# Kernel optimization log

Hardware: AMD Instinct MI355X
Metric: run time of the kernel (lower is better)

## Reference

```python
import jax, jax.numpy as jnp
import numpy as np

STRIDES = (8, 16, 32)
REG_MAX = 16
NUM_CLASSES = 80
FMP = ((80, 80), (40, 40), (20, 20))  # 640x640 input / strides


def _anchors(h, w, stride):
    # torch.meshgrid([arange(h), arange(w)]) -> (y, x); stack [x, y]; +0.5; *stride
    ys, xs = jnp.meshgrid(jnp.arange(h, dtype=jnp.float32),
                          jnp.arange(w, dtype=jnp.float32), indexing='ij')
    return (jnp.stack([xs, ys], axis=-1).reshape(-1, 2) + 0.5) * stride  # [H*W, 2]


def _level(cls_feat, reg_feat, cls_w, cls_b, reg_w, reg_b, stride):
    B, _, H, W = cls_feat.shape
    M = H * W
    # 1x1 convs as channel contractions, directly producing NHWC layout
    cls_pred = jnp.einsum('bchw,oc->bhwo', cls_feat, cls_w) + cls_b  # [B,H,W,nc]
    reg_pred = jnp.einsum('bchw,oc->bhwo', reg_feat, reg_w) + reg_b  # [B,H,W,4*reg_max]
    cls_pred = cls_pred.reshape(B, M, NUM_CLASSES)
    reg_pred = reg_pred.reshape(B, M, 4, REG_MAX)
    # DFL: softmax over reg_max bins, project with linspace(0, reg_max, reg_max)
    proj = jnp.linspace(0.0, float(REG_MAX), REG_MAX)
    reg = jnp.einsum('bmfr,r->bmf', jax.nn.softmax(reg_pred, axis=-1), proj)  # [B,M,4]
    anch = _anchors(H, W, stride)  # [M,2], broadcasts over B
    box = jnp.concatenate([anch - reg[..., :2] * stride,
                           anch + reg[..., 2:] * stride], axis=-1)  # [B,M,4]
    return jnp.concatenate([jax.nn.sigmoid(cls_pred), box], axis=-1)  # [B,M,nc+4]


def setup_inputs() -> dict:
    key = jax.random.key(0)
    ks = jax.random.split(key, 18)
    d = {}
    for i, (h, w) in enumerate(FMP):
        d[f'cls_feat{i}'] = jax.random.normal(ks[i], (16, 256, h, w), dtype=jnp.float32)
        d[f'reg_feat{i}'] = jax.random.normal(ks[3 + i], (16, 256, h, w), dtype=jnp.float32)
        d[f'cls_w{i}'] = jax.random.normal(ks[6 + i], (NUM_CLASSES, 256), dtype=jnp.float32) * 0.02
        d[f'cls_b{i}'] = jax.random.normal(ks[9 + i], (NUM_CLASSES,), dtype=jnp.float32) * 0.02
        d[f'reg_w{i}'] = jax.random.normal(ks[12 + i], (4 * REG_MAX, 256), dtype=jnp.float32) * 0.02
        d[f'reg_b{i}'] = jax.random.normal(ks[15 + i], (4 * REG_MAX,), dtype=jnp.float32) * 0.02
    return d


def reference(cls_feat0, cls_feat1, cls_feat2,
              reg_feat0, reg_feat1, reg_feat2,
              cls_w0, cls_w1, cls_w2, cls_b0, cls_b1, cls_b2,
              reg_w0, reg_w1, reg_w2, reg_b0, reg_b1, reg_b2):
    cls_feats = (cls_feat0, cls_feat1, cls_feat2)
    reg_feats = (reg_feat0, reg_feat1, reg_feat2)
    cls_ws = (cls_w0, cls_w1, cls_w2)
    cls_bs = (cls_b0, cls_b1, cls_b2)
    reg_ws = (reg_w0, reg_w1, reg_w2)
    reg_bs = (reg_b0, reg_b1, reg_b2)
    outs = [_level(cls_feats[l], reg_feats[l], cls_ws[l], cls_bs[l],
                   reg_ws[l], reg_bs[l], STRIDES[l]) for l in range(3)]
    return jnp.concatenate(outs, axis=1)  # [B, 8400, nc+4]
```

## Files before the change

kernel.cpp:

```cpp
#include <hip/hip_runtime.h>
#include <hip/hip_bf16.h>
#include <cstdint>

typedef float v4f __attribute__((ext_vector_type(4)));
typedef float v2f __attribute__((ext_vector_type(2)));

#define LVL_WSTRIDE 40960
#define BIASPAD_OFF 122880

__global__ __launch_bounds__(256) void prep_weights(
    const float* __restrict__ cw0, const float* __restrict__ cb0,
    const float* __restrict__ rw0, const float* __restrict__ rb0,
    const float* __restrict__ cw1, const float* __restrict__ cb1,
    const float* __restrict__ rw1, const float* __restrict__ rb1,
    const float* __restrict__ cw2, const float* __restrict__ cb2,
    const float* __restrict__ rw2, const float* __restrict__ rb2,
    float* __restrict__ ws)
{
  const int gid = blockIdx.x * 256 + threadIdx.x;
  const float* cws[3] = {cw0, cw1, cw2};
  const float* cbs[3] = {cb0, cb1, cb2};
  const float* rws[3] = {rw0, rw1, rw2};
  const float* rbs[3] = {rb0, rb1, rb2};
  if (gid < 3 * LVL_WSTRIDE) {
    const int l = gid / LVL_WSTRIDE;
    const int rem = gid - l * LVL_WSTRIDE;
    const int c = rem / 160;
    const int j = rem - c * 160;
    float v = 0.f;
    if (j < 96) {
      const int g = j / 12, q = j - g * 12;
      if (q < 10) v = cws[l][(g * 10 + q) * 256 + c];
    } else {
      v = rws[l][(j - 96) * 256 + c];
    }
    ws[gid] = v;
  } else if (gid < 3 * LVL_WSTRIDE + 480) {
    const int i = gid - 3 * LVL_WSTRIDE;
    const int l = i / 160;
    const int j = i - l * 160;
    float v = 0.f;
    if (j < 96) {
      const int g = j / 12, q = j - g * 12;
      if (q < 10) v = cbs[l][g * 10 + q];
    } else {
      v = rbs[l][j - 96];
    }
    ws[BIASPAD_OFF + i] = v;
  }
}

__global__ __launch_bounds__(256, 3) void head_kernel(
    const float* __restrict__ cf0, const float* __restrict__ rf0,
    const float* __restrict__ cf1, const float* __restrict__ rf1,
    const float* __restrict__ cf2, const float* __restrict__ rf2,
    const float* __restrict__ ws, float* __restrict__ out)
{
  __shared__ float pool[11008];
  float* const As     = pool;
  float* const Bs     = pool + 1024;
  float* const rstage = pool + 1792;
  float* const dstage = pool + 10496;
  float* const ostage = pool;

  const int t = threadIdx.x;
  const int bid = blockIdx.x;

  int l, r;
  if (bid < 800)       { l = 0; r = bid; }
  else if (bid < 1008) { l = 1; r = bid - 800; }
  else                 { l = 2; r = bid - 1008; }

  const int tiles = (l == 0) ? 50 : (l == 1) ? 13 : 4;
  const int M     = (l == 0) ? 6400 : (l == 1) ? 1600 : 400;
  const int W     = (l == 0) ? 80 : (l == 1) ? 40 : 20;
  const int moff  = (l == 0) ? 0 : (l == 1) ? 6400 : 8000;
  const float sv  = (float)(8 << l);

  const int b    = r / tiles;
  const int tile = r - b * tiles;
  const int m0   = tile * 128;

  const float* const cf   = (l == 0) ? cf0 : (l == 1) ? cf1 : cf2;
  const float* const rf   = (l == 0) ? rf0 : (l == 1) ? rf1 : rf2;
  const float* const wT   = ws + l * LVL_WSTRIDE;
  const float* const bias = ws + BIASPAD_OFF + l * 160;

  const int mg  = t & 31;
  const int og  = t >> 5;
  const int mg4 = mg * 4;

  const int mclamp = min(m0 + mg4, M - 4);

  float accR[4][8];
#pragma unroll
  for (int i = 0; i < 4; ++i)
#pragma unroll
    for (int j = 0; j < 8; ++j) accR[i][j] = 0.f;

  const float* const featR = rf + (size_t)b * 256 * (size_t)M;
  for (int ks = 0; ks < 32; ++ks) {
    const int k = ks * 8;
    const v4f av = *(const v4f*)(featR + (size_t)(k + og) * M + mclamp);
    v4f bv;
    if (t < 128) {
      const int cc = t >> 4, jj = (t & 15) * 4;
      bv = *(const v4f*)(wT + (k + cc) * 160 + 96 + jj);
    }
    __syncthreads();
    *(v4f*)&As[t * 4] = av;
    if (t < 128) *(v4f*)&Bs[t * 4] = bv;
    __syncthreads();
#pragma unroll
    for (int cc = 0; cc < 8; ++cc) {
      const v4f a  = *(const v4f*)&As[cc * 128 + mg4];
      const v4f b0 = *(const v4f*)&Bs[cc * 64 + og * 8];
      const v4f b1 = *(const v4f*)&Bs[cc * 64 + og * 8 + 4];
#pragma unroll
      for (int i = 0; i < 4; ++i) {
#pragma unroll
        for (int j = 0; j < 4; ++j) {
          accR[i][j]     += a[i] * b0[j];
          accR[i][j + 4] += a[i] * b1[j];
        }
      }
    }
  }
  __syncthreads();

#pragma unroll
  for (int i = 0; i < 4; ++i) {
    const int m = mg4 + i;
#pragma unroll
    for (int j = 0; j < 8; ++j)
      rstage[m * 68 + og * 8 + j] = accR[i][j] + bias[96 + og * 8 + j];
  }
  __syncthreads();

  float dv0 = 0.f, dv1 = 0.f;
#pragma unroll
  for (int it = 0; it < 2; ++it) {
    const int tau = t + it * 256;
    const int m = tau >> 2, f = tau & 3;
    const float* xp = &rstage[m * 68 + f * 16];
    float x[16];
    *(v4f*)&x[0]  = *(const v4f*)(xp);
    *(v4f*)&x[4]  = *(const v4f*)(xp + 4);
    *(v4f*)&x[8]  = *(const v4f*)(xp + 8);
    *(v4f*)&x[12] = *(const v4f*)(xp + 12);
    float mx = x[0];
#pragma unroll
    for (int q = 1; q < 16; ++q) mx = fmaxf(mx, x[q]);
    float s = 0.f, d = 0.f;
#pragma unroll
    for (int q = 0; q < 16; ++q) {
      const float e = __expf(x[q] - mx);
      s += e;
      d += e * (float)q;
    }
    const float res = d * (16.f / 15.f) / s;
    if (it == 0) dv0 = res; else dv1 = res;
  }
  dstage[t]       = dv0;
  dstage[t + 256] = dv1;
  __syncthreads();

  float bx0 = 0.f, by0 = 0.f, bx1 = 0.f, by1 = 0.f;
  if (t < 128) {
    const v4f dd = *(const v4f*)&dstage[t * 4];
    const int mglob = m0 + t;
    const int hh = mglob / W;
    const int wcol = mglob - hh * W;
    const float ax = ((float)wcol + 0.5f) * sv;
    const float ay = ((float)hh + 0.5f) * sv;
    bx0 = ax - dd[0] * sv;
    by0 = ay - dd[1] * sv;
    bx1 = ax + dd[2] * sv;
    by1 = ay + dd[3] * sv;
  }

  float accC[4][10];
#pragma unroll
  for (int i = 0; i < 4; ++i)
#pragma unroll
    for (int j = 0; j < 10; ++j) accC[i][j] = 0.f;

  const float* const featC = cf + (size_t)b * 256 * (size_t)M;
  for (int ks = 0; ks < 32; ++ks) {
    const int k = ks * 8;
    const v4f av = *(const v4f*)(featC + (size_t)(k + og) * M + mclamp);
    v4f bv;
    if (t < 192) {
      const int cc = t / 24;
      const int jj = (t - cc * 24) * 4;
      bv = *(const v4f*)(wT + (k + cc) * 160 + jj);
    }
    __syncthreads();
    *(v4f*)&As[t * 4] = av;
    if (t < 192) *(v4f*)&Bs[t * 4] = bv;
    __syncthreads();
#pragma unroll
    for (int cc = 0; cc < 8; ++cc) {
      const v4f a  = *(const v4f*)&As[cc * 128 + mg4];
      const v4f b0 = *(const v4f*)&Bs[cc * 96 + og * 12];
      const v4f b1 = *(const v4f*)&Bs[cc * 96 + og * 12 + 4];
      const v2f b2 = *(const v2f*)&Bs[cc * 96 + og * 12 + 8];
#pragma unroll
      for (int i = 0; i < 4; ++i) {
#pragma unroll
        for (int j = 0; j < 4; ++j) {
          accC[i][j]     += a[i] * b0[j];
          accC[i][j + 4] += a[i] * b1[j];
        }
        accC[i][8] += a[i] * b2[0];
        accC[i][9] += a[i] * b2[1];
      }
    }
  }
  __syncthreads();

#pragma unroll
  for (int i = 0; i < 4; ++i) {
    const int m = mg4 + i;
#pragma unroll
    for (int j = 0; j < 10; ++j) {
      const float z = accC[i][j] + bias[og * 12 + j];
      ostage[m * 84 + og * 10 + j] = 1.f / (1.f + __expf(-z));
    }
  }
  if (t < 128) {
    v4f bb; bb[0] = bx0; bb[1] = by0; bb[2] = bx1; bb[3] = by1;
    *(v4f*)&ostage[t * 84 + 80] = bb;
  }
  __syncthreads();

  float* const obase = out + ((size_t)b * 8400 + moff + m0) * 84;
#pragma unroll
  for (int i = 0; i < 21; ++i) {
    const int p  = i * 256 + t;
    const int fe = p * 2;
    const int m  = fe / 84;
    if (m0 + m < M) {
      *(v2f*)(obase + fe) = *(const v2f*)&ostage[fe];
    }
  }
}

extern "C" void kernel_launch(void* const* d_in, const int* in_sizes, int n_in,
                              void* d_out, int out_size, void* d_ws, size_t ws_size,
                              hipStream_t stream) {
  const float* cf[3]; const float* rff[3];
  const float* cw[3]; const float* cb[3];
  const float* rw[3]; const float* rb[3];
  for (int i = 0; i < 3; ++i) {
    cf[i]  = (const float*)d_in[i * 6 + 0];
    rff[i] = (const float*)d_in[i * 6 + 1];
    cw[i]  = (const float*)d_in[i * 6 + 2];
    cb[i]  = (const float*)d_in[i * 6 + 3];
    rw[i]  = (const float*)d_in[i * 6 + 4];
    rb[i]  = (const float*)d_in[i * 6 + 5];
  }
  float* ws = (float*)d_ws;
  float* o  = (float*)d_out;

  prep_weights<<<dim3(482), dim3(256), 0, stream>>>(
      cw[0], cb[0], rw[0], rb[0],
      cw[1], cb[1], rw[1], rb[1],
      cw[2], cb[2], rw[2], rb[2], ws);

  head_kernel<<<dim3(1072), dim3(256), 0, stream>>>(
      cf[0], rff[0], cf[1], rff[1], cf[2], rff[2], ws, o);
}
```

Baseline: 399.7 us.

## Use split-bf16 MFMA for 1x1 conv GEMMs with shuffle-based DFL softmax

Replaces the scalar FP32 FMA GEMMs with MFMA 16x16x32 bf16 instructions. Each FP32 operand is split into hi and lo bf16 parts and three MFMAs per tile keep accuracy close to FP32. Weights are pre-swizzled into MFMA lane order by the prep kernel. Feature loads are software-prefetched one k-slice ahead, and the DFL softmax now runs in registers with cross-lane shuffles, which removes the LDS staging passes. The cost is extra ALU work to pack the hi/lo parts and a small precision loss from the dropped lo*lo term. The kernel is likely memory-bound on roughly 300MB of feature reads.

Result: faster. 352.9 us (-11.7%).

```diff
diff --git a/kernel.cpp b/kernel.cpp
--- a/kernel.cpp
+++ b/kernel.cpp
@@ -4,9 +4,30 @@
 
 typedef float v4f __attribute__((ext_vector_type(4)));
 typedef float v2f __attribute__((ext_vector_type(2)));
-
-#define LVL_WSTRIDE 40960
-#define BIASPAD_OFF 122880
+typedef short s8v __attribute__((ext_vector_type(8)));
+typedef unsigned short u16;
+
+#define WSB_LVL     73728
+#define WSB_CLS_SZ  40960
+#define BIAS_OFF_B  442368
+
+__device__ __forceinline__ u16 bfbits(float x) {
+  return __builtin_bit_cast(u16, __float2bfloat16(x));
+}
+__device__ __forceinline__ float bff(u16 b) {
+  return __builtin_bit_cast(float, ((unsigned int)b) << 16);
+}
+__device__ __forceinline__ unsigned int packhi(float a, float b) {
+  return (unsigned int)bfbits(a) | ((unsigned int)bfbits(b) << 16);
+}
+__device__ __forceinline__ unsigned int packlo(float a, float b) {
+  const float ra = a - bff(bfbits(a));
+  const float rb = b - bff(bfbits(b));
+  return packhi(ra, rb);
+}
+__device__ __forceinline__ v4f mfma16(s8v a, s8v b, v4f c) {
+  return __builtin_amdgcn_mfma_f32_16x16x32_bf16(a, b, c, 0, 0, 0);
+}
 
 __global__ __launch_bounds__(256) void prep_weights(
     const float* __restrict__ cw0, const float* __restrict__ cb0,
@@ -15,38 +36,103 @@
     const float* __restrict__ rw1, const float* __restrict__ rb1,
     const float* __restrict__ cw2, const float* __restrict__ cb2,
     const float* __restrict__ rw2, const float* __restrict__ rb2,
-    float* __restrict__ ws)
+    void* __restrict__ wsv)
 {
+  u16* wsB = (u16*)wsv;
+  float* biasf = (float*)((char*)wsv + BIAS_OFF_B);
   const int gid = blockIdx.x * 256 + threadIdx.x;
   const float* cws[3] = {cw0, cw1, cw2};
   const float* cbs[3] = {cb0, cb1, cb2};
   const float* rws[3] = {rw0, rw1, rw2};
   const float* rbs[3] = {rb0, rb1, rb2};
-  if (gid < 3 * LVL_WSTRIDE) {
-    const int l = gid / LVL_WSTRIDE;
-    const int rem = gid - l * LVL_WSTRIDE;
-    const int c = rem / 160;
-    const int j = rem - c * 160;
-    float v = 0.f;
-    if (j < 96) {
-      const int g = j / 12, q = j - g * 12;
-      if (q < 10) v = cws[l][(g * 10 + q) * 256 + c];
-    } else {
-      v = rws[l][(j - 96) * 256 + c];
-    }
-    ws[gid] = v;
-  } else if (gid < 3 * LVL_WSTRIDE + 480) {
-    const int i = gid - 3 * LVL_WSTRIDE;
-    const int l = i / 160;
-    const int j = i - l * 160;
-    float v = 0.f;
-    if (j < 96) {
-      const int g = j / 12, q = j - g * 12;
-      if (q < 10) v = cbs[l][g * 10 + q];
-    } else {
-      v = rbs[l][j - 96];
-    }
-    ws[BIASPAD_OFF + i] = v;
+
+  if (gid < 3 * WSB_LVL) {
+    const int l = gid / WSB_LVL;
+    int r = gid - l * WSB_LVL;
+    const bool cls = r < WSB_CLS_SZ;
+    if (!cls) r -= WSB_CLS_SZ;
+    const int j    = r & 7;
+    const int lane = (r >> 3) & 63;
+    const int hl   = (r >> 9) & 1;
+    int nt, ks;
+    if (cls) { const int v = r >> 10; nt = v % 5; ks = v / 5; }
+    else     { nt = (r >> 10) & 3; ks = r >> 12; }
+    const int o = nt * 16 + (lane & 15);
+    const int k = ks * 32 + (lane >> 4) * 8 + j;
+    const float* w = cls ? cws[l] : rws[l];
+    const float v = w[o * 256 + k];
+    u16 bits;
+    if (hl == 0) bits = bfbits(v);
+    else         bits = bfbits(v - bff(bfbits(v)));
+    wsB[gid] = bits;
+  } else if (gid < 3 * WSB_LVL + 432) {
+    const int i = gid - 3 * WSB_LVL;
+    const int l = i / 144;
+    const int o = i - l * 144;
+    biasf[l * 144 + o] = (o < 80) ? cbs[l][o] : rbs[l][o - 80];
+  }
+}
+
+template<int NT>
+__device__ __forceinline__ void gemm_accum(const float* __restrict__ feat,
+                                           const u16* __restrict__ wB,
+                                           u16* Abuf, const int t,
+                                           const int m0, const int M,
+                                           v4f (&acc)[2][NT])
+{
+  const int kp   = t & 15;
+  const int mq0  = t >> 4;
+  const int mmA  = min(m0 + mq0 * 4, M - 4);
+  const int mmB  = min(m0 + (mq0 + 16) * 4, M - 4);
+  const int lane   = t & 63;
+  const int lane15 = lane & 15;
+  const int kg     = lane >> 4;
+  const int mbase  = (t >> 6) * 32;
+  unsigned int* AbufW = (unsigned int*)Abuf;
+  const int w0 = (mq0 * 4) * 36 + kp;
+  const int w1 = ((mq0 + 16) * 4) * 36 + kp;
+
+  v4f r0a = *(const v4f*)(feat + (size_t)(2 * kp) * M + mmA);
+  v4f r0b = *(const v4f*)(feat + (size_t)(2 * kp + 1) * M + mmA);
+  v4f r1a = *(const v4f*)(feat + (size_t)(2 * kp) * M + mmB);
+  v4f r1b = *(const v4f*)(feat + (size_t)(2 * kp + 1) * M + mmB);
+
+#pragma unroll
+  for (int ks = 0; ks < 8; ++ks) {
+#pragma unroll
+    for (int j = 0; j < 4; ++j) {
+      AbufW[w0 + j * 36]      = packhi(r0a[j], r0b[j]);
+      AbufW[w0 + j * 36 + 16] = packlo(r0a[j], r0b[j]);
+      AbufW[w1 + j * 36]      = packhi(r1a[j], r1b[j]);
+      AbufW[w1 + j * 36 + 16] = packlo(r1a[j], r1b[j]);
+    }
+    if (ks < 7) {
+      const size_t ko = (size_t)((ks + 1) * 32 + 2 * kp) * M;
+      r0a = *(const v4f*)(feat + ko + mmA);
+      r0b = *(const v4f*)(feat + ko + M + mmA);
+      r1a = *(const v4f*)(feat + ko + mmB);
+      r1b = *(const v4f*)(feat + ko + M + mmB);
+    }
+    __syncthreads();
+    const u16* arow0 = Abuf + (mbase + lane15) * 72 + kg * 8;
+    const u16* arow1 = Abuf + (mbase + 16 + lane15) * 72 + kg * 8;
+    const s8v ahi0 = *(const s8v*)(arow0);
+    const s8v alo0 = *(const s8v*)(arow0 + 32);
+    const s8v ahi1 = *(const s8v*)(arow1);
+    const s8v alo1 = *(const s8v*)(arow1 + 32);
+#pragma unroll
+    for (int nt = 0; nt < NT; ++nt) {
+      const u16* bp = wB + (size_t)((ks * NT + nt) * 2) * 512 + lane * 8;
+      const s8v bhi = *(const s8v*)(bp);
+      const s8v blo = *(const s8v*)(bp + 512);
+      acc[0][nt] = mfma16(ahi0, bhi, acc[0][nt]);
+      acc[0][nt] = mfma16(ahi0, blo, acc[0][nt]);
+      acc[0][nt] = mfma16(alo0, bhi, acc[0][nt]);
+      acc[1][nt] = mfma16(ahi1, bhi, acc[1][nt]);
+      acc[1][nt] = mfma16(ahi1, blo, acc[1][nt]);
+      acc[1][nt] = mfma16(alo1, bhi, acc[1][nt]);
+    }
+    __syncthreads();
   }
 }
 
@@ -54,16 +140,17 @@
     const float* __restrict__ cf0, const float* __restrict__ rf0,
     const float* __restrict__ cf1, const float* __restrict__ rf1,
     const float* __restrict__ cf2, const float* __restrict__ rf2,
-    const float* __restrict__ ws, float* __restrict__ out)
+    const void* __restrict__ wsv, float* __restrict__ out)
 {
-  __shared__ float pool[11008];
-  float* const As     = pool;
-  float* const Bs     = pool + 1024;
-  float* const rstage = pool + 1792;
-  float* const dstage = pool + 10496;
-  float* const ostage = pool;
-
-  const int t = threadIdx.x;
+  __shared__ __align__(16) char smem[45056];
+  u16*  Abuf     = (u16*)smem;
+  float* ostage   = (float*)smem;
+  float* boxstage = (float*)(smem + 43008);
+
+  const u16*  wsB   = (const u16*)wsv;
+  const float* biasf = (const float*)((const char*)wsv + BIAS_OFF_B);
+
+  const int t   = threadIdx.x;
   const int bid = blockIdx.x;
 
   int l, r;
@@ -81,155 +168,98 @@
   const int tile = r - b * tiles;
   const int m0   = tile * 128;
 
-  const float* const cf   = (l == 0) ? cf0 : (l == 1) ? cf1 : cf2;
-  const float* const rf   = (l == 0) ? rf0 : (l == 1) ? rf1 : rf2;
-  const float* const wT   = ws + l * LVL_WSTRIDE;
-  const float* const bias = ws + BIASPAD_OFF + l * 160;
-
-  const int mg  = t & 31;
-  const int og  = t >> 5;
-  const int mg4 = mg * 4;
-
-  const int mclamp = min(m0 + mg4, M - 4);
-
-  float accR[4][8];
-#pragma unroll
-  for (int i = 0; i < 4; ++i)
-#pragma unroll
-    for (int j = 0; j < 8; ++j) accR[i][j] = 0.f;
-
-  const float* const featR = rf + (size_t)b * 256 * (size_t)M;
-  for (int ks = 0; ks < 32; ++ks) {
-    const int k = ks * 8;
-    const v4f av = *(const v4f*)(featR + (size_t)(k + og) * M + mclamp);
-    v4f bv;
-    if (t < 128) {
-      const int cc = t >> 4, jj = (t & 15) * 4;
-      bv = *(const v4f*)(wT + (k + cc) * 160 + 96 + jj);
-    }
-    __syncthreads();
-    *(v4f*)&As[t * 4] = av;
-    if (t < 128) *(v4f*)&Bs[t * 4] = bv;
-    __syncthreads();
-#pragma unroll
-    for (int cc = 0; cc < 8; ++cc) {
-      const v4f a  = *(const v4f*)&As[cc * 128 + mg4];
-      const v4f b0 = *(const v4f*)&Bs[cc * 64 + og * 8];
-      const v4f b1 = *(const v4f*)&Bs[cc * 64 + og * 8 + 4];
-#pragma unroll
-      for (int i = 0; i < 4; ++i) {
-#pragma unroll
-        for (int j = 0; j < 4; ++j) {
-          accR[i][j]     += a[i] * b0[j];
-          accR[i][j + 4] += a[i] * b1[j];
-        }
+  const float* cfL = (l == 0) ? cf0 : (l == 1) ? cf1 : cf2;
+  const float* rfL = (l == 0) ? rf0 : (l == 1) ? rf1 : rf2;
+  const float* featR = rfL + (size_t)b * 256 * (size_t)M;
+  const float* featC = cfL + (size_t)b * 256 * (size_t)M;
+  const u16* wBcls = wsB + l * WSB_LVL;
+  const u16* wBreg = wsB + l * WSB_LVL + WSB_CLS_SZ;
+  const int loff = l * 144;
+
+  const int lane   = t & 63;
+  const int lane15 = lane & 15;
+  const int kg     = lane >> 4;
+  const int mbase  = (t >> 6) * 32;
+
+  v4f accR[2][4];
+#pragma unroll
+  for (int mr = 0; mr < 2; ++mr)
+#pragma unroll
+    for (int nt = 0; nt < 4; ++nt) accR[mr][nt] = (v4f){0.f, 0.f, 0.f, 0.f};
+  gemm_accum<4>(featR, wBreg, Abuf, t, m0, M, accR);
+
+  float bR[4];
+#pragma unroll
+  for (int f = 0; f < 4; ++f) bR[f] = biasf[loff + 80 + f * 16 + lane15];
+
+  float d[2][4][4];
+#pragma unroll
+  for (int mr = 0; mr < 2; ++mr) {
+#pragma unroll
+    for (int f = 0; f < 4; ++f) {
+#pragma unroll
+      for (int rr = 0; rr < 4; ++rr) {
+        const float xx = accR[mr][f][rr] + bR[f];
+        float mx = xx;
+        mx = fmaxf(mx, __shfl_xor(mx, 1));
+        mx = fmaxf(mx, __shfl_xor(mx, 2));
+        mx = fmaxf(mx, __shfl_xor(mx, 4));
+        mx = fmaxf(mx, __shfl_xor(mx, 8));
+        const float e = __expf(xx - mx);
+        float s = e, wq = e * (float)lane15;
+        s += __shfl_xor(s, 1); wq += __shfl_xor(wq, 1);
+        s += __shfl_xor(s, 2); wq += __shfl_xor(wq, 2);
+        s += __shfl_xor(s, 4); wq += __shfl_xor(wq, 4);
+        s += __shfl_xor(s, 8); wq += __shfl_xor(wq, 8);
+        d[mr][f][rr] = wq * (16.0f / 15.0f) / s;
       }
     }
   }
-  __syncthreads();
-
-#pragma unroll
-  for (int i = 0; i < 4; ++i) {
-    const int m = mg4 + i;
-#pragma unroll
-    for (int j = 0; j < 8; ++j)
-      rstage[m * 68 + og * 8 + j] = accR[i][j] + bias[96 + og * 8 + j];
-  }
-  __syncthreads();
-
-  float dv0 = 0.f, dv1 = 0.f;
-#pragma unroll
-  for (int it = 0; it < 2; ++it) {
-    const int tau = t + it * 256;
-    const int m = tau >> 2, f = tau & 3;
-    const float* xp = &rstage[m * 68 + f * 16];
-    float x[16];
-    *(v4f*)&x[0]  = *(const v4f*)(xp);
-    *(v4f*)&x[4]  = *(const v4f*)(xp + 4);
-    *(v4f*)&x[8]  = *(const v4f*)(xp + 8);
-    *(v4f*)&x[12] = *(const v4f*)(xp + 12);
-    float mx = x[0];
-#pragma unroll
-    for (int q = 1; q < 16; ++q) mx = fmaxf(mx, x[q]);
-    float s = 0.f, d = 0.f;
-#pragma unroll
-    for (int q = 0; q < 16; ++q) {
-      const float e = __expf(x[q] - mx);
-      s += e;
-      d += e * (float)q;
-    }
-    const float res = d * (16.f / 15.f) / s;
-    if (it == 0) dv0 = res; else dv1 = res;
-  }
-  dstage[t]       = dv0;
-  dstage[t + 256] = dv1;
-  __syncthreads();
-
-  float bx0 = 0.f, by0 = 0.f, bx1 = 0.f, by1 = 0.f;
+
+#pragma unroll
+  for (int mr = 0; mr < 2; ++mr) {
+#pragma unroll
+    for (int rr = 0; rr < 4; ++rr) {
+      if (lane15 == mr * 4 + rr) {
+        const int pl = mbase + mr * 16 + kg * 4 + rr;
+        const int pg = m0 + pl;
+        const int hh = pg / W;
+        const int wc = pg - hh * W;
+        const float ax = ((float)wc + 0.5f) * sv;
+        const float ay = ((float)hh + 0.5f) * sv;
+        v4f bb;
+        bb[0] = ax - d[mr][0][rr] * sv;
+        bb[1] = ay - d[mr][1][rr] * sv;
+        bb[2] = ax + d[mr][2][rr] * sv;
+        bb[3] = ay + d[mr][3][rr] * sv;
+        *(v4f*)&boxstage[pl * 4] = bb;
+      }
+    }
+  }
+
+  v4f accC[2][5];
+#pragma unroll
+  for (int mr = 0; mr < 2; ++mr)
+#pragma unroll
+    for (int nt = 0; nt < 5; ++nt) accC[mr][nt] = (v4f){0.f, 0.f, 0.f, 0.f};
+  gemm_accum<5>(featC, wBcls, Abuf, t, m0, M, accC);
+
+  float bC[5];
+#pragma unroll
+  for (int nt = 0; nt < 5; ++nt) bC[nt] = biasf[loff + nt * 16 + lane15];
+
+#pragma unroll
+  for (int mr = 0; mr < 2; ++mr)
+#pragma unroll
+    for (int nt = 0; nt < 5; ++nt)
+#pragma unroll
+      for (int rr = 0; rr < 4; ++rr) {
+        const float z = accC[mr][nt][rr] + bC[nt];
+        ostage[(mbase + mr * 16 + kg * 4 + rr) * 84 + nt * 16 + lane15] =
+            1.f / (1.f + __expf(-z));
+      }
   if (t < 128) {
-    const v4f dd = *(const v4f*)&dstage[t * 4];
-    const int mglob = m0 + t;
-    const int hh = mglob / W;
-    const int wcol = mglob - hh * W;
-    const float ax = ((float)wcol + 0.5f) * sv;
-    const float ay = ((float)hh + 0.5f) * sv;
-    bx0 = ax - dd[0] * sv;
-    by0 = ay - dd[1] * sv;
-    bx1 = ax + dd[2] * sv;
-    by1 = ay + dd[3] * sv;
-  }
-
-  float accC[4][10];
-#pragma unroll
-  for (int i = 0; i < 4; ++i)
-#pragma unroll
-    for (int j = 0; j < 10; ++j) accC[i][j] = 0.f;
-
-  const float* const featC = cf + (size_t)b * 256 * (size_t)M;
-  for (int ks = 0; ks < 32; ++ks) {
-    const int k = ks * 8;
-    const v4f av = *(const v4f*)(featC + (size_t)(k + og) * M + mclamp);
-    v4f bv;
-    if (t < 192) {
-      const int cc = t / 24;
-      const int jj = (t - cc * 24) * 4;
-      bv = *(const v4f*)(wT + (k + cc) * 160 + jj);
-    }
-    __syncthreads();
-    *(v4f*)&As[t * 4] = av;
-    if (t < 192) *(v4f*)&Bs[t * 4] = bv;
-    __syncthreads();
-#pragma unroll
-    for (int cc = 0; cc < 8; ++cc) {
-      const v4f a  = *(const v4f*)&As[cc * 128 + mg4];
-      const v4f b0 = *(const v4f*)&Bs[cc * 96 + og * 12];
-      const v4f b1 = *(const v4f*)&Bs[cc * 96 + og * 12 + 4];
-      const v2f b2 = *(const v2f*)&Bs[cc * 96 + og * 12 + 8];
-#pragma unroll
-      for (int i = 0; i < 4; ++i) {
-#pragma unroll
-        for (int j = 0; j < 4; ++j) {
-          accC[i][j]     += a[i] * b0[j];
-          accC[i][j + 4] += a[i] * b1[j];
-        }
-        accC[i][8] += a[i] * b2[0];
-        accC[i][9] += a[i] * b2[1];
-      }
-    }
-  }
-  __syncthreads();
-
-#pragma unroll
-  for (int i = 0; i < 4; ++i) {
-    const int m = mg4 + i;
-#pragma unroll
-    for (int j = 0; j < 10; ++j) {
-      const float z = accC[i][j] + bias[og * 12 + j];
-      ostage[m * 84 + og * 10 + j] = 1.f / (1.f + __expf(-z));
-    }
-  }
-  if (t < 128) {
-    v4f bb; bb[0] = bx0; bb[1] = by0; bb[2] = bx1; bb[3] = by1;
+    const v4f bb = *(const v4f*)&boxstage[t * 4];
     *(v4f*)&ostage[t * 84 + 80] = bb;
   }
   __syncthreads();
@@ -260,14 +290,13 @@
     rw[i]  = (const float*)d_in[i * 6 + 4];
     rb[i]  = (const float*)d_in[i * 6 + 5];
   }
-  float* ws = (float*)d_ws;
-  float* o  = (float*)d_out;
-
-  prep_weights<<<dim3(482), dim3(256), 0, stream>>>(
+  float* o = (float*)d_out;
+
+  prep_weights<<<dim3(866), dim3(256), 0, stream>>>(
       cw[0], cb[0], rw[0], rb[0],
       cw[1], cb[1], rw[1], rb[1],
-      cw[2], cb[2], rw[2], rb[2], ws);
+      cw[2], cb[2], rw[2], rb[2], d_ws);
 
   head_kernel<<<dim3(1072), dim3(256), 0, stream>>>(
-      cf[0], rff[0], cf[1], rff[1], cf[2], rff[2], ws, o);
-}
+      cf[0], rff[0], cf[1], rff[1], cf[2], rff[2], d_ws, o);
+}
```
